# Kernel tuning notes

Hardware: AMD Instinct MI355X
Metric: run time of the kernel (lower is better)

## Reference

```python
import jax, jax.numpy as jnp
import numpy as np

N_NODES = 50000
N_EDGES = 800000
N_GRAPHS = 2048


def setup_inputs() -> dict:
    key = jax.random.key(0)
    ks = jax.random.split(key, 16)
    x = jax.random.normal(ks[0], (N_NODES, 32), dtype=jnp.float32)
    edge_index = jax.random.randint(ks[1], (2, N_EDGES), 0, N_NODES, dtype=jnp.int64)
    batch = jnp.sort(jax.random.randint(ks[2], (N_NODES,), 0, N_GRAPHS, dtype=jnp.int64))
    def w(k, fi, fo):
        return jax.random.normal(k, (fi, fo), dtype=jnp.float32) * (1.0 / np.sqrt(fi))
    return {
        "x": x, "edge_index": edge_index, "batch": batch,
        "W1": w(ks[3], 32, 64), "b1": jnp.zeros((64,), jnp.float32),
        "W2": w(ks[4], 64, 64), "b2": jnp.zeros((64,), jnp.float32),
        "W3": w(ks[5], 64, 64), "b3": jnp.zeros((64,), jnp.float32),
        "lw1": w(ks[6], 64, 64), "lb1": jnp.zeros((64,), jnp.float32),
        "lw2": w(ks[7], 64, 2), "lb2": jnp.zeros((2,), jnp.float32),
    }


def reference(x, edge_index, batch, W1, b1, W2, b2, W3, b3, lw1, lb1, lw2, lb2):
    N = x.shape[0]
    # GCNConv default: add self loops, symmetric normalization
    loops = jnp.arange(N, dtype=edge_index.dtype)
    src = jnp.concatenate([edge_index[0], loops])
    dst = jnp.concatenate([edge_index[1], loops])
    ones = jnp.ones_like(src, dtype=x.dtype)
    deg = jax.ops.segment_sum(ones, dst, num_segments=N)  # in-degree incl. self loops
    dinv = jnp.where(deg > 0, jax.lax.rsqrt(deg), 0.0)
    norm = dinv[src] * dinv[dst]  # [E+N]

    def gcn_relu(h, W, b):
        h = h @ W                                    # [N, F]
        msg = h[src] * norm[:, None]                 # gather + scale [E+N, F]
        out = jax.ops.segment_sum(msg, dst, num_segments=N) + b
        return jax.nn.relu(out)

    h = gcn_relu(x, W1, b1)
    h = gcn_relu(h, W2, b2)
    h = gcn_relu(h, W3, b3)

    # global_mean_pool over graph ids
    summed = jax.ops.segment_sum(h, batch, num_segments=N_GRAPHS)  # [G, F]
    counts = jax.ops.segment_sum(jnp.ones((N,), h.dtype), batch, num_segments=N_GRAPHS)
    pooled = summed / jnp.maximum(counts, 1.0)[:, None]

    # dropout is identity in eval mode
    out = jax.nn.relu(pooled @ lw1 + lb1) @ lw2 + lb2
    return out
```

## Files before the change

kernel.cpp:

```cpp
#include <hip/hip_runtime.h>

#define NN 50000
#define NE 800000
#define NG 2048
#define F 64

constexpr int SCAN_B = 256;
constexpr int NB = (NN + SCAN_B - 1) / SCAN_B;

typedef float f4 __attribute__((ext_vector_type(4)));

__global__ void deg_kernel(const int* __restrict__ dst, int* __restrict__ deg) {
    int e = blockIdx.x * 256 + threadIdx.x;
    if (e < NE) atomicAdd(&deg[dst[e]], 1);
}

__global__ void dinv_kernel(const int* __restrict__ deg, float* __restrict__ dinv) {
    int v = blockIdx.x * 256 + threadIdx.x;
    if (v < NN) dinv[v] = rsqrtf((float)(deg[v] + 1));
}

__global__ void scalex_kernel(const float4* __restrict__ x4, const float* __restrict__ dinv,
                              float4* __restrict__ xd4) {
    int i = blockIdx.x * 256 + threadIdx.x;
    if (i < NN * 8) {
        int v = i >> 3;
        float d = dinv[v];
        float4 a = x4[i];
        a.x *= d; a.y *= d; a.z *= d; a.w *= d;
        xd4[i] = a;
    }
}

__global__ void scan1_kernel(const int* __restrict__ deg, int* __restrict__ bsums) {
    __shared__ int s[256];
    int t = threadIdx.x, i = blockIdx.x * 256 + t;
    s[t] = (i < NN) ? deg[i] : 0;
    __syncthreads();
    for (int off = 128; off > 0; off >>= 1) {
        if (t < off) s[t] += s[t + off];
        __syncthreads();
    }
    if (t == 0) bsums[blockIdx.x] = s[0];
}

__global__ void scan2_kernel(int* __restrict__ bsums, int* __restrict__ rowptr) {
    __shared__ int s[256];
    int t = threadIdx.x;
    int v = (t < NB) ? bsums[t] : 0;
    s[t] = v;
    __syncthreads();
    for (int off = 1; off < 256; off <<= 1) {
        int x = (t >= off) ? s[t - off] : 0;
        __syncthreads();
        s[t] += x;
        __syncthreads();
    }
    if (t < NB) bsums[t] = s[t] - v;
    if (t == 0) rowptr[NN] = NE;
}

__global__ void scan3_kernel(const int* __restrict__ deg, const int* __restrict__ bsums,
                             int* __restrict__ rowptr, int* __restrict__ cursor) {
    __shared__ int s[256];
    int t = threadIdx.x, i = blockIdx.x * 256 + t;
    int v = (i < NN) ? deg[i] : 0;
    s[t] = v;
    __syncthreads();
    for (int off = 1; off < 256; off <<= 1) {
        int x = (t >= off) ? s[t - off] : 0;
        __syncthreads();
        s[t] += x;
        __syncthreads();
    }
    if (i < NN) {
        int rp = bsums[blockIdx.x] + s[t] - v;
        rowptr[i] = rp;
        cursor[i] = rp;
    }
}

__global__ void fill_kernel(const int* __restrict__ src, const int* __restrict__ dst,
                            int* __restrict__ cursor, int* __restrict__ col) {
    int e = blockIdx.x * 256 + threadIdx.x;
    if (e < NE) {
        int slot = atomicAdd(&cursor[dst[e]], 1);
        col[slot] = src[e];
    }
}

__global__ void agg32_kernel(const f4* __restrict__ g4, const int* __restrict__ rowptr,
                             const int* __restrict__ col, const float* __restrict__ dinv,
                             float* __restrict__ out) {
    int lane = threadIdx.x & 63;
    int v = blockIdx.x * 4 + (threadIdx.x >> 6);
    int slot = lane >> 3, fq = lane & 7;
    int beg = rowptr[v], end = rowptr[v + 1];
    f4 acc = {0.f, 0.f, 0.f, 0.f};
    for (int base = beg; base < end; base += 32) {
        f4 a[4];
        float w[4];
#pragma unroll
        for (int j = 0; j < 4; ++j) {
            int e = base + slot + j * 8;
            int ce = (e < end) ? e : (end - 1);
            w[j] = (e < end) ? 1.f : 0.f;
            int u = col[ce];
            a[j] = g4[(long)u * 8 + fq];
        }
#pragma unroll
        for (int j = 0; j < 4; ++j) acc += w[j] * a[j];
    }
#pragma unroll
    for (int m = 8; m < 64; m <<= 1) {
        acc.x += __shfl_xor(acc.x, m);
        acc.y += __shfl_xor(acc.y, m);
        acc.z += __shfl_xor(acc.z, m);
        acc.w += __shfl_xor(acc.w, m);
    }
    f4 self = g4[(long)v * 8 + fq];
    float d = dinv[v];
    acc = d * (acc + self);
    if (slot < 4) {
        float comp = (slot == 0) ? acc.x : (slot == 1) ? acc.y : (slot == 2) ? acc.z : acc.w;
        out[(long)v * 32 + 4 * fq + slot] = comp;
    }
}

template <bool POOL>
__global__ void agg4_kernel(const f4* __restrict__ g4, const int* __restrict__ rowptr,
                            const int* __restrict__ col, const float* __restrict__ dinv,
                            const f4* __restrict__ bias4, float* __restrict__ out,
                            const int* __restrict__ batch, float* __restrict__ pooled,
                            float* __restrict__ counts) {
    int lane = threadIdx.x & 63;
    int v = blockIdx.x * 4 + (threadIdx.x >> 6);
    int slot = lane >> 4, fq = lane & 15;
    int beg = rowptr[v], end = rowptr[v + 1];
    f4 acc = {0.f, 0.f, 0.f, 0.f};
    for (int base = beg; base < end; base += 32) {
        f4 a[8];
        float w[8];
#pragma unroll
        for (int j = 0; j < 8; ++j) {
            int e = base + slot + j * 4;
            int ce = (e < end) ? e : (end - 1);
            w[j] = (e < end) ? 1.f : 0.f;
            int u = col[ce];
            a[j] = g4[(long)u * 16 + fq];
        }
#pragma unroll
        for (int j = 0; j < 8; ++j) acc += w[j] * a[j];
    }
#pragma unroll
    for (int m = 16; m < 64; m <<= 1) {
        acc.x += __shfl_xor(acc.x, m);
        acc.y += __shfl_xor(acc.y, m);
        acc.z += __shfl_xor(acc.z, m);
        acc.w += __shfl_xor(acc.w, m);
    }
    f4 self = g4[(long)v * 16 + fq];
    float d = dinv[v];
    f4 bb = bias4[fq];
    f4 hv;
    hv.x = fmaxf(fmaf(d, acc.x + self.x, bb.x), 0.f);
    hv.y = fmaxf(fmaf(d, acc.y + self.y, bb.y), 0.f);
    hv.z = fmaxf(fmaf(d, acc.z + self.z, bb.z), 0.f);
    hv.w = fmaxf(fmaf(d, acc.w + self.w, bb.w), 0.f);
    float comp = (slot == 0) ? hv.x : (slot == 1) ? hv.y : (slot == 2) ? hv.z : hv.w;
    if (POOL) {
        int b = batch[v];
        atomicAdd(&pooled[(long)b * F + 4 * fq + slot], comp);
        if (lane == 0) atomicAdd(&counts[b], 1.0f);
    } else {
        out[(long)v * F + 4 * fq + slot] = comp;
    }
}

template <int K, bool RELU_BIAS>
__global__ void gemm_kernel(const float* __restrict__ in, const float* __restrict__ W,
                            const float* __restrict__ bias, const float* __restrict__ dinv,
                            float* __restrict__ out) {
    __shared__ float Ws[K * F];
    int t = threadIdx.x;
#pragma unroll
    for (int i = 0; i < K * F / 256; ++i) Ws[i * 256 + t] = W[i * 256 + t];
    __syncthreads();
    int f = t & 63;
    int slot = __builtin_amdgcn_readfirstlane(t >> 6);
    int n0 = blockIdx.x * 16 + slot;
    float acc0 = 0.f, acc1 = 0.f, acc2 = 0.f, acc3 = 0.f;
    const float* r0 = in + (long)n0 * K;
    const float* r1 = r0 + 4 * K;
    const float* r2 = r0 + 8 * K;
    const float* r3 = r0 + 12 * K;
#pragma unroll
    for (int k = 0; k < K; ++k) {
        float w = Ws[k * F + f];
        acc0 = fmaf(r0[k], w, acc0);
        acc1 = fmaf(r1[k], w, acc1);
        acc2 = fmaf(r2[k], w, acc2);
        acc3 = fmaf(r3[k], w, acc3);
    }
    if (RELU_BIAS) {
        float b = bias[f];
        out[(long)n0 * F + f]        = fmaxf(acc0 + b, 0.f);
        out[(long)(n0 + 4) * F + f]  = fmaxf(acc1 + b, 0.f);
        out[(long)(n0 + 8) * F + f]  = fmaxf(acc2 + b, 0.f);
        out[(long)(n0 + 12) * F + f] = fmaxf(acc3 + b, 0.f);
    } else {
        out[(long)n0 * F + f]        = dinv[n0] * acc0;
        out[(long)(n0 + 4) * F + f]  = dinv[n0 + 4] * acc1;
        out[(long)(n0 + 8) * F + f]  = dinv[n0 + 8] * acc2;
        out[(long)(n0 + 12) * F + f] = dinv[n0 + 12] * acc3;
    }
}

__global__ void head_kernel(const float* __restrict__ pooled, const float* __restrict__ counts,
                            const float* __restrict__ lw1, const float* __restrict__ lb1,
                            const float* __restrict__ lw2, const float* __restrict__ lb2,
                            float* __restrict__ out) {
    __shared__ float p[F];
    __shared__ float hid[F];
    int gid = blockIdx.x, t = threadIdx.x;
    float cnt = fmaxf(counts[gid], 1.0f);
    p[t] = pooled[(long)gid * F + t] / cnt;
    __syncthreads();
    float acc = lb1[t];
#pragma unroll 8
    for (int k = 0; k < F; ++k) acc = fmaf(p[k], lw1[k * F + t], acc);
    hid[t] = fmaxf(acc, 0.f);
    __syncthreads();
    if (t < 2) {
        float a = lb2[t];
#pragma unroll 8
        for (int k = 0; k < F; ++k) a = fmaf(hid[k], lw2[k * 2 + t], a);
        out[(long)gid * 2 + t] = a;
    }
}

extern "C" void kernel_launch(void* const* d_in, const int* in_sizes, int n_in,
                              void* d_out, int out_size, void* d_ws, size_t ws_size,
                              hipStream_t stream) {
    const float* x    = (const float*)d_in[0];
    const int*   ei   = (const int*)d_in[1];
    const int*   bat  = (const int*)d_in[2];
    const float* W1   = (const float*)d_in[3];
    const float* b1   = (const float*)d_in[4];
    const float* W2   = (const float*)d_in[5];
    const float* b2   = (const float*)d_in[6];
    const float* W3   = (const float*)d_in[7];
    const float* b3   = (const float*)d_in[8];
    const float* lw1  = (const float*)d_in[9];
    const float* lb1  = (const float*)d_in[10];
    const float* lw2  = (const float*)d_in[11];
    const float* lb2  = (const float*)d_in[12];
    float* out = (float*)d_out;

    const int* src = ei;
    const int* dst = ei + NE;

    char* ws = (char*)d_ws;
    size_t off = 0;
    auto carve = [&](size_t bytes) {
        void* p = ws + off;
        off += (bytes + 255) & ~(size_t)255;
        return p;
    };
    int*   deg     = (int*)carve(NN * 4);
    float* dinv    = (float*)carve(NN * 4);
    int*   rowptr  = (int*)carve((NN + 1) * 4);
    int*   cursor  = (int*)carve(NN * 4);
    int*   bsums   = (int*)carve(256 * 4);
    int*   col     = (int*)carve((size_t)NE * 4);
    float* xd      = (float*)carve((size_t)NN * 32 * 4);
    float* sbuf    = (float*)carve((size_t)NN * 32 * 4);
    float* bufA    = (float*)carve((size_t)NN * F * 4);
    float* bufB    = (float*)carve((size_t)NN * F * 4);
    float* pooled  = (float*)carve((size_t)NG * F * 4 + NG * 4);
    float* counts  = pooled + (size_t)NG * F;

    hipMemsetAsync(deg, 0, NN * 4, stream);
    hipMemsetAsync(pooled, 0, ((size_t)NG * F + NG) * 4, stream);

    deg_kernel<<<(NE + 255) / 256, 256, 0, stream>>>(dst, deg);
    dinv_kernel<<<NB, 256, 0, stream>>>(deg, dinv);
    scalex_kernel<<<(NN * 8 + 255) / 256, 256, 0, stream>>>((const float4*)x, dinv, (float4*)xd);
    scan1_kernel<<<NB, 256, 0, stream>>>(deg, bsums);
    scan2_kernel<<<1, 256, 0, stream>>>(bsums, rowptr);
    scan3_kernel<<<NB, 256, 0, stream>>>(deg, bsums, rowptr, cursor);
    fill_kernel<<<(NE + 255) / 256, 256, 0, stream>>>(src, dst, cursor, col);

    const int gridN = (NN + 3) / 4;
    const int gridG = NN / 16;

    agg32_kernel<<<gridN, 256, 0, stream>>>((const f4*)xd, rowptr, col, dinv, sbuf);
    gemm_kernel<32, true><<<gridG, 256, 0, stream>>>(sbuf, W1, b1, dinv, bufA);

    gemm_kernel<64, false><<<gridG, 256, 0, stream>>>(bufA, W2, nullptr, dinv, bufB);
    agg4_kernel<false><<<gridN, 256, 0, stream>>>((const f4*)bufB, rowptr, col, dinv,
                                                  (const f4*)b2, bufA,
                                                  nullptr, nullptr, nullptr);
    gemm_kernel<64, false><<<gridG, 256, 0, stream>>>(bufA, W3, nullptr, dinv, bufB);
    agg4_kernel<true><<<gridN, 256, 0, stream>>>((const f4*)bufB, rowptr, col, dinv,
                                                 (const f4*)b3, nullptr,
                                                 bat, pooled, counts);
    head_kernel<<<NG, 64, 0, stream>>>(pooled, counts, lw1, lb1, lw2, lb2, out);
}
```

Before: 324.2 us.

## Split aggregation feature dimension across blocks to process more edges per wave

The aggregation kernels now split each node's feature vector across several blocks: halves for the 32-wide layer and quarters for the 64-wide layers. Each wave covers 16 edges in parallel, with each lane loading one float4 of one feature slice. Block indices are interleaved so that blocks sharing the same node group run close together and can reuse cached col/rowptr data. This exposes more edge-level parallelism and more gathers in flight, at the cost of re-reading col indices several times and launching several times as many blocks.

```diff
diff --git a/kernel.cpp b/kernel.cpp
--- a/kernel.cpp
+++ b/kernel.cpp
@@ -92,38 +92,40 @@
 __global__ void agg32_kernel(const f4* __restrict__ g4, const int* __restrict__ rowptr,
                              const int* __restrict__ col, const float* __restrict__ dinv,
                              float* __restrict__ out) {
-    int lane = threadIdx.x & 63;
-    int v = blockIdx.x * 4 + (threadIdx.x >> 6);
-    int slot = lane >> 3, fq = lane & 7;
+    int tid = threadIdx.x, lane = tid & 63;
+    int bi = blockIdx.x;
+    int h = (bi & 7) >> 2;
+    int vg = ((bi >> 3) << 2) | (bi & 3);
+    int v = vg * 4 + (tid >> 6);
+    int slot = lane >> 2, fj = lane & 3;
     int beg = rowptr[v], end = rowptr[v + 1];
     f4 acc = {0.f, 0.f, 0.f, 0.f};
     for (int base = beg; base < end; base += 32) {
-        f4 a[4];
-        float w[4];
-#pragma unroll
-        for (int j = 0; j < 4; ++j) {
-            int e = base + slot + j * 8;
+        f4 a[2];
+        float w[2];
+#pragma unroll
+        for (int j = 0; j < 2; ++j) {
+            int e = base + slot + j * 16;
             int ce = (e < end) ? e : (end - 1);
             w[j] = (e < end) ? 1.f : 0.f;
             int u = col[ce];
-            a[j] = g4[(long)u * 8 + fq];
+            a[j] = g4[(long)u * 8 + h * 4 + fj];
         }
-#pragma unroll
-        for (int j = 0; j < 4; ++j) acc += w[j] * a[j];
-    }
-#pragma unroll
-    for (int m = 8; m < 64; m <<= 1) {
+        acc += w[0] * a[0] + w[1] * a[1];
+    }
+#pragma unroll
+    for (int m = 4; m < 64; m <<= 1) {
         acc.x += __shfl_xor(acc.x, m);
         acc.y += __shfl_xor(acc.y, m);
         acc.z += __shfl_xor(acc.z, m);
         acc.w += __shfl_xor(acc.w, m);
     }
-    f4 self = g4[(long)v * 8 + fq];
+    f4 self = g4[(long)v * 8 + h * 4 + fj];
     float d = dinv[v];
     acc = d * (acc + self);
     if (slot < 4) {
         float comp = (slot == 0) ? acc.x : (slot == 1) ? acc.y : (slot == 2) ? acc.z : acc.w;
-        out[(long)v * 32 + 4 * fq + slot] = comp;
+        out[(long)v * 32 + h * 16 + fj * 4 + slot] = comp;
     }
 }
 
@@ -133,48 +135,52 @@
                             const f4* __restrict__ bias4, float* __restrict__ out,
                             const int* __restrict__ batch, float* __restrict__ pooled,
                             float* __restrict__ counts) {
-    int lane = threadIdx.x & 63;
-    int v = blockIdx.x * 4 + (threadIdx.x >> 6);
-    int slot = lane >> 4, fq = lane & 15;
+    int tid = threadIdx.x, lane = tid & 63;
+    int bi = blockIdx.x;
+    int q = (bi & 7) >> 1;
+    int vg = ((bi >> 3) << 1) | (bi & 1);
+    int v = vg * 4 + (tid >> 6);
+    int slot = lane >> 2, fj = lane & 3;
     int beg = rowptr[v], end = rowptr[v + 1];
     f4 acc = {0.f, 0.f, 0.f, 0.f};
     for (int base = beg; base < end; base += 32) {
-        f4 a[8];
-        float w[8];
-#pragma unroll
-        for (int j = 0; j < 8; ++j) {
-            int e = base + slot + j * 4;
+        f4 a[2];
+        float w[2];
+#pragma unroll
+        for (int j = 0; j < 2; ++j) {
+            int e = base + slot + j * 16;
             int ce = (e < end) ? e : (end - 1);
             w[j] = (e < end) ? 1.f : 0.f;
             int u = col[ce];
-            a[j] = g4[(long)u * 16 + fq];
+            a[j] = g4[(long)u * 16 + q * 4 + fj];
         }
-#pragma unroll
-        for (int j = 0; j < 8; ++j) acc += w[j] * a[j];
-    }
-#pragma unroll
-    for (int m = 16; m < 64; m <<= 1) {
+        acc += w[0] * a[0] + w[1] * a[1];
+    }
+#pragma unroll
+    for (int m = 4; m < 64; m <<= 1) {
         acc.x += __shfl_xor(acc.x, m);
         acc.y += __shfl_xor(acc.y, m);
         acc.z += __shfl_xor(acc.z, m);
         acc.w += __shfl_xor(acc.w, m);
     }
-    f4 self = g4[(long)v * 16 + fq];
+    f4 self = g4[(long)v * 16 + q * 4 + fj];
     float d = dinv[v];
-    f4 bb = bias4[fq];
+    f4 bb = bias4[q * 4 + fj];
     f4 hv;
     hv.x = fmaxf(fmaf(d, acc.x + self.x, bb.x), 0.f);
     hv.y = fmaxf(fmaf(d, acc.y + self.y, bb.y), 0.f);
     hv.z = fmaxf(fmaf(d, acc.z + self.z, bb.z), 0.f);
     hv.w = fmaxf(fmaf(d, acc.w + self.w, bb.w), 0.f);
-    float comp = (slot == 0) ? hv.x : (slot == 1) ? hv.y : (slot == 2) ? hv.z : hv.w;
-    if (POOL) {
-        int b = batch[v];
-        atomicAdd(&pooled[(long)b * F + 4 * fq + slot], comp);
-        if (lane == 0) atomicAdd(&counts[b], 1.0f);
-    } else {
-        out[(long)v * F + 4 * fq + slot] = comp;
-    }
+    if (slot < 4) {
+        float comp = (slot == 0) ? hv.x : (slot == 1) ? hv.y : (slot == 2) ? hv.z : hv.w;
+        int feat = q * 16 + fj * 4 + slot;
+        if (POOL) {
+            atomicAdd(&pooled[(long)batch[v] * F + feat], comp);
+        } else {
+            out[(long)v * F + feat] = comp;
+        }
+    }
+    if (POOL && q == 0 && lane == 0) atomicAdd(&counts[batch[v]], 1.0f);
 }
 
 template <int K, bool RELU_BIAS>
@@ -291,18 +297,19 @@
     scan3_kernel<<<NB, 256, 0, stream>>>(deg, bsums, rowptr, cursor);
     fill_kernel<<<(NE + 255) / 256, 256, 0, stream>>>(src, dst, cursor, col);
 
-    const int gridN = (NN + 3) / 4;
+    const int gridH = 2 * (NN / 4);
+    const int gridQ = 4 * (NN / 4);
     const int gridG = NN / 16;
 
-    agg32_kernel<<<gridN, 256, 0, stream>>>((const f4*)xd, rowptr, col, dinv, sbuf);
+    agg32_kernel<<<gridH, 256, 0, stream>>>((const f4*)xd, rowptr, col, dinv, sbuf);
     gemm_kernel<32, true><<<gridG, 256, 0, stream>>>(sbuf, W1, b1, dinv, bufA);
 
     gemm_kernel<64, false><<<gridG, 256, 0, stream>>>(bufA, W2, nullptr, dinv, bufB);
-    agg4_kernel<false><<<gridN, 256, 0, stream>>>((const f4*)bufB, rowptr, col, dinv,
+    agg4_kernel<false><<<gridQ, 256, 0, stream>>>((const f4*)bufB, rowptr, col, dinv,
                                                   (const f4*)b2, bufA,
                                                   nullptr, nullptr, nullptr);
     gemm_kernel<64, false><<<gridG, 256, 0, stream>>>(bufA, W3, nullptr, dinv, bufB);
-    agg4_kernel<true><<<gridN, 256, 0, stream>>>((const f4*)bufB, rowptr, col, dinv,
+    agg4_kernel<true><<<gridQ, 256, 0, stream>>>((const f4*)bufB, rowptr, col, dinv,
                                                  (const f4*)b3, nullptr,
                                                  bat, pooled, counts);
     head_kernel<<<NG, 64, 0, stream>>>(pooled, counts, lw1, lb1, lw2, lb2, out);
```

Result: slower. 443.4 us (+36.8%).

## Fuse CSR build and preprocessing into one cooperative kernel with grid syncs

Applied to the files above, without the earlier changes.

Replaces two memsets and seven small preprocessing kernels (degree count, dinv, x scaling, three-pass scan, CSR fill) with one cooperative kernel of 1024 blocks that separates the phases with grid-wide syncs. The aim is to remove per-launch overhead and the idle gaps between tiny dependent kernels. In exchange, every phase runs on a fixed, smaller grid, grid.sync barriers add cost, and cooperative launch requires all 1024 blocks to be resident at once.

```diff
diff --git a/kernel.cpp b/kernel.cpp
--- a/kernel.cpp
+++ b/kernel.cpp
@@ -1,91 +1,97 @@
 #include <hip/hip_runtime.h>
+#include <hip/hip_cooperative_groups.h>
+
+namespace cg = cooperative_groups;
 
 #define NN 50000
 #define NE 800000
 #define NG 2048
 #define F 64
 
-constexpr int SCAN_B = 256;
-constexpr int NB = (NN + SCAN_B - 1) / SCAN_B;
+constexpr int NB = (NN + 255) / 256;
+constexpr int CG = 1024;
+constexpr int CT = 256;
 
 typedef float f4 __attribute__((ext_vector_type(4)));
 
-__global__ void deg_kernel(const int* __restrict__ dst, int* __restrict__ deg) {
-    int e = blockIdx.x * 256 + threadIdx.x;
-    if (e < NE) atomicAdd(&deg[dst[e]], 1);
-}
-
-__global__ void dinv_kernel(const int* __restrict__ deg, float* __restrict__ dinv) {
-    int v = blockIdx.x * 256 + threadIdx.x;
-    if (v < NN) dinv[v] = rsqrtf((float)(deg[v] + 1));
-}
-
-__global__ void scalex_kernel(const float4* __restrict__ x4, const float* __restrict__ dinv,
-                              float4* __restrict__ xd4) {
-    int i = blockIdx.x * 256 + threadIdx.x;
-    if (i < NN * 8) {
+__global__ void __launch_bounds__(CT, 8)
+csr_build(const int* __restrict__ src, const int* __restrict__ dst,
+          const float4* __restrict__ x4,
+          int* __restrict__ deg, float* __restrict__ dinv, float4* __restrict__ xd4,
+          int* __restrict__ rowptr, int* __restrict__ cursor, int* __restrict__ col,
+          int* __restrict__ partial, float* __restrict__ pooled_counts) {
+    cg::grid_group grid = cg::this_grid();
+    __shared__ int s[CT];
+    const int t = threadIdx.x, b = blockIdx.x;
+    const int gtid = b * CT + t, gsz = CG * CT;
+
+    for (int i = gtid; i < NN; i += gsz) deg[i] = 0;
+    for (int i = gtid; i < NG * F + NG; i += gsz) pooled_counts[i] = 0.f;
+    grid.sync();
+
+    for (int e = gtid; e < NE; e += gsz) atomicAdd(&deg[dst[e]], 1);
+    grid.sync();
+
+    for (int i = gtid; i < NN; i += gsz) dinv[i] = rsqrtf((float)(deg[i] + 1));
+    for (int i = gtid; i < NN * 8; i += gsz) {
         int v = i >> 3;
-        float d = dinv[v];
+        float d = rsqrtf((float)(deg[v] + 1));
         float4 a = x4[i];
         a.x *= d; a.y *= d; a.z *= d; a.w *= d;
         xd4[i] = a;
     }
-}
-
-__global__ void scan1_kernel(const int* __restrict__ deg, int* __restrict__ bsums) {
-    __shared__ int s[256];
-    int t = threadIdx.x, i = blockIdx.x * 256 + t;
-    s[t] = (i < NN) ? deg[i] : 0;
-    __syncthreads();
-    for (int off = 128; off > 0; off >>= 1) {
-        if (t < off) s[t] += s[t + off];
-        __syncthreads();
-    }
-    if (t == 0) bsums[blockIdx.x] = s[0];
-}
-
-__global__ void scan2_kernel(int* __restrict__ bsums, int* __restrict__ rowptr) {
-    __shared__ int s[256];
-    int t = threadIdx.x;
-    int v = (t < NB) ? bsums[t] : 0;
-    s[t] = v;
-    __syncthreads();
-    for (int off = 1; off < 256; off <<= 1) {
-        int x = (t >= off) ? s[t - off] : 0;
-        __syncthreads();
-        s[t] += x;
-        __syncthreads();
-    }
-    if (t < NB) bsums[t] = s[t] - v;
-    if (t == 0) rowptr[NN] = NE;
-}
-
-__global__ void scan3_kernel(const int* __restrict__ deg, const int* __restrict__ bsums,
-                             int* __restrict__ rowptr, int* __restrict__ cursor) {
-    __shared__ int s[256];
-    int t = threadIdx.x, i = blockIdx.x * 256 + t;
-    int v = (i < NN) ? deg[i] : 0;
-    s[t] = v;
-    __syncthreads();
-    for (int off = 1; off < 256; off <<= 1) {
-        int x = (t >= off) ? s[t - off] : 0;
-        __syncthreads();
-        s[t] += x;
-        __syncthreads();
-    }
-    if (i < NN) {
-        int rp = bsums[blockIdx.x] + s[t] - v;
-        rowptr[i] = rp;
-        cursor[i] = rp;
-    }
-}
-
-__global__ void fill_kernel(const int* __restrict__ src, const int* __restrict__ dst,
-                            int* __restrict__ cursor, int* __restrict__ col) {
-    int e = blockIdx.x * 256 + threadIdx.x;
-    if (e < NE) {
+    for (int c = b; c < NB; c += CG) {
+        int i = c * 256 + t;
+        s[t] = (i < NN) ? deg[i] : 0;
+        __syncthreads();
+        for (int off = 128; off > 0; off >>= 1) {
+            if (t < off) s[t] += s[t + off];
+            __syncthreads();
+        }
+        if (t == 0) partial[c] = s[0];
+        __syncthreads();
+    }
+    grid.sync();
+
+    if (b == 0) {
+        int v = (t < NB) ? partial[t] : 0;
+        s[t] = v;
+        __syncthreads();
+        for (int off = 1; off < 256; off <<= 1) {
+            int x = (t >= off) ? s[t - off] : 0;
+            __syncthreads();
+            s[t] += x;
+            __syncthreads();
+        }
+        if (t < NB) partial[t] = s[t] - v;
+        if (t == 0) rowptr[NN] = NE;
+    }
+    grid.sync();
+
+    for (int c = b; c < NB; c += CG) {
+        int i = c * 256 + t;
+        int v = (i < NN) ? deg[i] : 0;
+        s[t] = v;
+        __syncthreads();
+        for (int off = 1; off < 256; off <<= 1) {
+            int x = (t >= off) ? s[t - off] : 0;
+            __syncthreads();
+            s[t] += x;
+            __syncthreads();
+        }
+        if (i < NN) {
+            int rp = partial[c] + s[t] - v;
+            rowptr[i] = rp;
+            cursor[i] = rp;
+        }
+        __syncthreads();
+    }
+    grid.sync();
+
+    for (int e = gtid; e < NE; e += gsz) {
+        int sv = src[e];
         int slot = atomicAdd(&cursor[dst[e]], 1);
-        col[slot] = src[e];
+        col[slot] = sv;
     }
 }
 
@@ -257,9 +263,6 @@
     const float* lb2  = (const float*)d_in[12];
     float* out = (float*)d_out;
 
-    const int* src = ei;
-    const int* dst = ei + NE;
-
     char* ws = (char*)d_ws;
     size_t off = 0;
     auto carve = [&](size_t bytes) {
@@ -271,7 +274,7 @@
     float* dinv    = (float*)carve(NN * 4);
     int*   rowptr  = (int*)carve((NN + 1) * 4);
     int*   cursor  = (int*)carve(NN * 4);
-    int*   bsums   = (int*)carve(256 * 4);
+    int*   partial = (int*)carve(256 * 4);
     int*   col     = (int*)carve((size_t)NE * 4);
     float* xd      = (float*)carve((size_t)NN * 32 * 4);
     float* sbuf    = (float*)carve((size_t)NN * 32 * 4);
@@ -280,18 +283,19 @@
     float* pooled  = (float*)carve((size_t)NG * F * 4 + NG * 4);
     float* counts  = pooled + (size_t)NG * F;
 
-    hipMemsetAsync(deg, 0, NN * 4, stream);
-    hipMemsetAsync(pooled, 0, ((size_t)NG * F + NG) * 4, stream);
-
-    deg_kernel<<<(NE + 255) / 256, 256, 0, stream>>>(dst, deg);
-    dinv_kernel<<<NB, 256, 0, stream>>>(deg, dinv);
-    scalex_kernel<<<(NN * 8 + 255) / 256, 256, 0, stream>>>((const float4*)x, dinv, (float4*)xd);
-    scan1_kernel<<<NB, 256, 0, stream>>>(deg, bsums);
-    scan2_kernel<<<1, 256, 0, stream>>>(bsums, rowptr);
-    scan3_kernel<<<NB, 256, 0, stream>>>(deg, bsums, rowptr, cursor);
-    fill_kernel<<<(NE + 255) / 256, 256, 0, stream>>>(src, dst, cursor, col);
-
-    const int gridN = (NN + 3) / 4;
+    {
+        const int* srcp = ei;
+        const int* dstp = ei + NE;
+        const float4* x4p = (const float4*)x;
+        float4* xd4p = (float4*)xd;
+        void* args[] = {(void*)&srcp, (void*)&dstp, (void*)&x4p,
+                        (void*)&deg, (void*)&dinv, (void*)&xd4p,
+                        (void*)&rowptr, (void*)&cursor, (void*)&col,
+                        (void*)&partial, (void*)&pooled};
+        hipLaunchCooperativeKernel((void*)csr_build, dim3(CG), dim3(CT), args, 0, stream);
+    }
+
+    const int gridN = NN / 4;
     const int gridG = NN / 16;
 
     agg32_kernel<<<gridN, 256, 0, stream>>>((const f4*)xd, rowptr, col, dinv, sbuf);
```

New measurement: 809.8 us. +149.8%, slower.

## Split 64-feature aggregation into two 32-feature halves with blocked node batches

Applied to the files above, without the earlier changes.

The GEMM epilogue now writes its output as two separate 32-feature planes. The aggregation kernel processes one half at a time, with each wave handling 16 consecutive nodes and the block index interleaving halves, so each gathered row is 128 bytes and the working set per half is smaller and more cache-friendly. The dinv computation is folded into the x-scaling kernel and the two scan phases are merged into one kernel, removing two launches. The trade-off is that the edge list is traversed twice, there are more pooling atomics, and the loop over nodes is serial within each wave.

```diff
diff --git a/kernel.cpp b/kernel.cpp
--- a/kernel.cpp
+++ b/kernel.cpp
@@ -5,8 +5,7 @@
 #define NG 2048
 #define F 64
 
-constexpr int SCAN_B = 256;
-constexpr int NB = (NN + SCAN_B - 1) / SCAN_B;
+constexpr int NB = (NN + 255) / 256;
 
 typedef float f4 __attribute__((ext_vector_type(4)));
 
@@ -15,17 +14,13 @@
     if (e < NE) atomicAdd(&deg[dst[e]], 1);
 }
 
-__global__ void dinv_kernel(const int* __restrict__ deg, float* __restrict__ dinv) {
-    int v = blockIdx.x * 256 + threadIdx.x;
-    if (v < NN) dinv[v] = rsqrtf((float)(deg[v] + 1));
-}
-
-__global__ void scalex_kernel(const float4* __restrict__ x4, const float* __restrict__ dinv,
-                              float4* __restrict__ xd4) {
+__global__ void scalex_kernel(const int* __restrict__ deg, const float4* __restrict__ x4,
+                              float* __restrict__ dinv, float4* __restrict__ xd4) {
     int i = blockIdx.x * 256 + threadIdx.x;
     if (i < NN * 8) {
         int v = i >> 3;
-        float d = dinv[v];
+        float d = rsqrtf((float)(deg[v] + 1));
+        if ((i & 7) == 0) dinv[v] = d;
         float4 a = x4[i];
         a.x *= d; a.y *= d; a.z *= d; a.w *= d;
         xd4[i] = a;
@@ -44,40 +39,36 @@
     if (t == 0) bsums[blockIdx.x] = s[0];
 }
 
-__global__ void scan2_kernel(int* __restrict__ bsums, int* __restrict__ rowptr) {
+__global__ void scan23_kernel(const int* __restrict__ deg, const int* __restrict__ bsums,
+                              int* __restrict__ rowptr, int* __restrict__ cursor) {
+    __shared__ int offs[256];
     __shared__ int s[256];
-    int t = threadIdx.x;
-    int v = (t < NB) ? bsums[t] : 0;
-    s[t] = v;
-    __syncthreads();
-    for (int off = 1; off < 256; off <<= 1) {
-        int x = (t >= off) ? s[t - off] : 0;
-        __syncthreads();
-        s[t] += x;
-        __syncthreads();
-    }
-    if (t < NB) bsums[t] = s[t] - v;
-    if (t == 0) rowptr[NN] = NE;
-}
-
-__global__ void scan3_kernel(const int* __restrict__ deg, const int* __restrict__ bsums,
-                             int* __restrict__ rowptr, int* __restrict__ cursor) {
-    __shared__ int s[256];
-    int t = threadIdx.x, i = blockIdx.x * 256 + t;
+    int t = threadIdx.x, blk = blockIdx.x;
+    offs[t] = (t < NB) ? bsums[t] : 0;
+    __syncthreads();
+    for (int o = 1; o < 256; o <<= 1) {
+        int x = (t >= o) ? offs[t - o] : 0;
+        __syncthreads();
+        offs[t] += x;
+        __syncthreads();
+    }
+    int chunk_off = (blk > 0) ? offs[blk - 1] : 0;
+    int i = blk * 256 + t;
     int v = (i < NN) ? deg[i] : 0;
     s[t] = v;
     __syncthreads();
-    for (int off = 1; off < 256; off <<= 1) {
-        int x = (t >= off) ? s[t - off] : 0;
+    for (int o = 1; o < 256; o <<= 1) {
+        int x = (t >= o) ? s[t - o] : 0;
         __syncthreads();
         s[t] += x;
         __syncthreads();
     }
     if (i < NN) {
-        int rp = bsums[blockIdx.x] + s[t] - v;
+        int rp = chunk_off + s[t] - v;
         rowptr[i] = rp;
         cursor[i] = rp;
     }
+    if (blk == 0 && t == 0) rowptr[NN] = NE;
 }
 
 __global__ void fill_kernel(const int* __restrict__ src, const int* __restrict__ dst,
@@ -128,52 +119,67 @@
 }
 
 template <bool POOL>
-__global__ void agg4_kernel(const f4* __restrict__ g4, const int* __restrict__ rowptr,
-                            const int* __restrict__ col, const float* __restrict__ dinv,
-                            const f4* __restrict__ bias4, float* __restrict__ out,
-                            const int* __restrict__ batch, float* __restrict__ pooled,
-                            float* __restrict__ counts) {
-    int lane = threadIdx.x & 63;
-    int v = blockIdx.x * 4 + (threadIdx.x >> 6);
-    int slot = lane >> 4, fq = lane & 15;
-    int beg = rowptr[v], end = rowptr[v + 1];
-    f4 acc = {0.f, 0.f, 0.f, 0.f};
-    for (int base = beg; base < end; base += 32) {
-        f4 a[8];
-        float w[8];
-#pragma unroll
-        for (int j = 0; j < 8; ++j) {
-            int e = base + slot + j * 4;
-            int ce = (e < end) ? e : (end - 1);
-            w[j] = (e < end) ? 1.f : 0.f;
-            int u = col[ce];
-            a[j] = g4[(long)u * 16 + fq];
+__global__ void agg4h_kernel(const f4* __restrict__ g, const int* __restrict__ rowptr,
+                             const int* __restrict__ col, const float* __restrict__ dinv,
+                             const f4* __restrict__ bias4, float* __restrict__ out,
+                             const int* __restrict__ batch, float* __restrict__ pooled,
+                             float* __restrict__ counts) {
+    int tid = threadIdx.x, lane = tid & 63, w = tid >> 6;
+    int bi = blockIdx.x;
+    int h = (bi & 7) >> 2;
+    int idx = ((bi >> 3) << 2) | (bi & 3);
+    int base = idx * 64 + w * 16;
+    if (base >= NN) return;
+    int slot = lane >> 3, fq = lane & 7;
+    const f4* gb = g + (long)h * NN * 8;
+    int li = base + ((lane < 17) ? lane : 16);
+    if (li > NN) li = NN;
+    int rpv = rowptr[li];
+#pragma unroll 1
+    for (int i = 0; i < 16; ++i) {
+        int v = base + i;
+        if (v >= NN) break;
+        int beg = __shfl(rpv, i), end = __shfl(rpv, i + 1);
+        f4 acc = {0.f, 0.f, 0.f, 0.f};
+        for (int b0 = beg; b0 < end; b0 += 32) {
+            f4 a[4];
+            float wt[4];
+#pragma unroll
+            for (int j = 0; j < 4; ++j) {
+                int e = b0 + slot + j * 8;
+                int ce = (e < end) ? e : (end - 1);
+                wt[j] = (e < end) ? 1.f : 0.f;
+                int u = col[ce];
+                a[j] = gb[(long)u * 8 + fq];
+            }
+#pragma unroll
+            for (int j = 0; j < 4; ++j) acc += wt[j] * a[j];
         }
 #pragma unroll
-        for (int j = 0; j < 8; ++j) acc += w[j] * a[j];
-    }
-#pragma unroll
-    for (int m = 16; m < 64; m <<= 1) {
-        acc.x += __shfl_xor(acc.x, m);
-        acc.y += __shfl_xor(acc.y, m);
-        acc.z += __shfl_xor(acc.z, m);
-        acc.w += __shfl_xor(acc.w, m);
-    }
-    f4 self = g4[(long)v * 16 + fq];
-    float d = dinv[v];
-    f4 bb = bias4[fq];
-    f4 hv;
-    hv.x = fmaxf(fmaf(d, acc.x + self.x, bb.x), 0.f);
-    hv.y = fmaxf(fmaf(d, acc.y + self.y, bb.y), 0.f);
-    hv.z = fmaxf(fmaf(d, acc.z + self.z, bb.z), 0.f);
-    hv.w = fmaxf(fmaf(d, acc.w + self.w, bb.w), 0.f);
-    float comp = (slot == 0) ? hv.x : (slot == 1) ? hv.y : (slot == 2) ? hv.z : hv.w;
-    if (POOL) {
-        int b = batch[v];
-        atomicAdd(&pooled[(long)b * F + 4 * fq + slot], comp);
-        if (lane == 0) atomicAdd(&counts[b], 1.0f);
-    } else {
-        out[(long)v * F + 4 * fq + slot] = comp;
+        for (int m = 8; m < 64; m <<= 1) {
+            acc.x += __shfl_xor(acc.x, m);
+            acc.y += __shfl_xor(acc.y, m);
+            acc.z += __shfl_xor(acc.z, m);
+            acc.w += __shfl_xor(acc.w, m);
+        }
+        f4 self = gb[(long)v * 8 + fq];
+        float d = dinv[v];
+        f4 bb = bias4[h * 8 + fq];
+        f4 hv;
+        hv.x = fmaxf(fmaf(d, acc.x + self.x, bb.x), 0.f);
+        hv.y = fmaxf(fmaf(d, acc.y + self.y, bb.y), 0.f);
+        hv.z = fmaxf(fmaf(d, acc.z + self.z, bb.z), 0.f);
+        hv.w = fmaxf(fmaf(d, acc.w + self.w, bb.w), 0.f);
+        if (slot < 4) {
+            float comp = (slot == 0) ? hv.x : (slot == 1) ? hv.y : (slot == 2) ? hv.z : hv.w;
+            int feat = h * 32 + fq * 4 + slot;
+            if (POOL) {
+                atomicAdd(&pooled[(long)batch[v] * F + feat], comp);
+            } else {
+                out[(long)v * F + feat] = comp;
+            }
+        }
+        if (POOL && h == 0 && lane == 0) atomicAdd(&counts[batch[v]], 1.0f);
     }
 }
 
@@ -209,10 +215,12 @@
         out[(long)(n0 + 8) * F + f]  = fmaxf(acc2 + b, 0.f);
         out[(long)(n0 + 12) * F + f] = fmaxf(acc3 + b, 0.f);
     } else {
-        out[(long)n0 * F + f]        = dinv[n0] * acc0;
-        out[(long)(n0 + 4) * F + f]  = dinv[n0 + 4] * acc1;
-        out[(long)(n0 + 8) * F + f]  = dinv[n0 + 8] * acc2;
-        out[(long)(n0 + 12) * F + f] = dinv[n0 + 12] * acc3;
+        int hh = f >> 5, fl = f & 31;
+        float* o = out + (long)hh * NN * 32 + fl;
+        o[(long)n0 * 32]        = dinv[n0] * acc0;
+        o[(long)(n0 + 4) * 32]  = dinv[n0 + 4] * acc1;
+        o[(long)(n0 + 8) * 32]  = dinv[n0 + 8] * acc2;
+        o[(long)(n0 + 12) * 32] = dinv[n0 + 12] * acc3;
     }
 }
 
@@ -284,26 +292,25 @@
     hipMemsetAsync(pooled, 0, ((size_t)NG * F + NG) * 4, stream);
 
     deg_kernel<<<(NE + 255) / 256, 256, 0, stream>>>(dst, deg);
-    dinv_kernel<<<NB, 256, 0, stream>>>(deg, dinv);
-    scalex_kernel<<<(NN * 8 + 255) / 256, 256, 0, stream>>>((const float4*)x, dinv, (float4*)xd);
+    scalex_kernel<<<(NN * 8 + 255) / 256, 256, 0, stream>>>(deg, (const float4*)x, dinv, (float4*)xd);
     scan1_kernel<<<NB, 256, 0, stream>>>(deg, bsums);
-    scan2_kernel<<<1, 256, 0, stream>>>(bsums, rowptr);
-    scan3_kernel<<<NB, 256, 0, stream>>>(deg, bsums, rowptr, cursor);
+    scan23_kernel<<<NB, 256, 0, stream>>>(deg, bsums, rowptr, cursor);
     fill_kernel<<<(NE + 255) / 256, 256, 0, stream>>>(src, dst, cursor, col);
 
-    const int gridN = (NN + 3) / 4;
+    const int gridN = NN / 4;
+    const int gridH = 196 * 8;
     const int gridG = NN / 16;
 
     agg32_kernel<<<gridN, 256, 0, stream>>>((const f4*)xd, rowptr, col, dinv, sbuf);
     gemm_kernel<32, true><<<gridG, 256, 0, stream>>>(sbuf, W1, b1, dinv, bufA);
 
     gemm_kernel<64, false><<<gridG, 256, 0, stream>>>(bufA, W2, nullptr, dinv, bufB);
-    agg4_kernel<false><<<gridN, 256, 0, stream>>>((const f4*)bufB, rowptr, col, dinv,
-                                                  (const f4*)b2, bufA,
-                                                  nullptr, nullptr, nullptr);
+    agg4h_kernel<false><<<gridH, 256, 0, stream>>>((const f4*)bufB, rowptr, col, dinv,
+                                                   (const f4*)b2, bufA,
+                                                   nullptr, nullptr, nullptr);
     gemm_kernel<64, false><<<gridG, 256, 0, stream>>>(bufA, W3, nullptr, dinv, bufB);
-    agg4_kernel<true><<<gridN, 256, 0, stream>>>((const f4*)bufB, rowptr, col, dinv,
-                                                 (const f4*)b3, nullptr,
-                                                 bat, pooled, counts);
+    agg4h_kernel<true><<<gridH, 256, 0, stream>>>((const f4*)bufB, rowptr, col, dinv,
+                                                  (const f4*)b3, nullptr,
+                                                  bat, pooled, counts);
     head_kernel<<<NG, 64, 0, stream>>>(pooled, counts, lw1, lb1, lw2, lb2, out);
 }
```

New measurement: 309.6 us. 1.05x faster.
